# Kernel optimization log

Hardware: AMD Instinct MI355X
Metric: run time of the kernel (lower is better)

Reference implementation:

```python
import jax, jax.numpy as jnp
import numpy as np
import math


def setup_inputs() -> dict:
    key = jax.random.key(0)
    k1, k2, k3 = jax.random.split(key, 3)
    b, h, s, d = 2, 16, 2048, 64
    q = jax.random.normal(k1, (b, h, s, d), dtype=jnp.float32)
    k = jax.random.normal(k2, (b, h, d, s), dtype=jnp.float32)  # pre-transposed as in the torch module
    v = jax.random.normal(k3, (b, h, s, d), dtype=jnp.float32)
    return {"q": q, "k": k, "v": v}


def reference(q, k, v):
    d = q.shape[-1]
    # unnormalized exp-attention, no max subtraction (faithful to source)
    p = jnp.exp(jnp.einsum('bhsd,bhdt->bhst', q, k) / math.sqrt(d))  # [b,h,s,s]
    attn = jnp.einsum('bhst,bhtd->bhsd', p, v)                        # [b,h,s,d]
    l = jnp.sum(p, axis=3, keepdims=True)                             # [b,h,s,1]
    return attn / l
```

## Files before the change

kernel.cpp:

```cpp
#include <hip/hip_runtime.h>

#define S_LEN 2048
#define D_DIM 64
#define BH 32
#define NN ((size_t)131072)

typedef short bf16x8 __attribute__((ext_vector_type(8)));
typedef float f32x16 __attribute__((ext_vector_type(16)));
typedef unsigned int u32x4 __attribute__((ext_vector_type(4)));

static __device__ __forceinline__ unsigned short f2bf(float x) {
  unsigned int u = __float_as_uint(x);
  u += 0x7fffu + ((u >> 16) & 1u);
  return (unsigned short)(u >> 16);
}
static __device__ __forceinline__ float bf2f(unsigned short h) {
  return __uint_as_float(((unsigned int)h) << 16);
}
static __device__ __forceinline__ void gll16(const void* g, void* l) {
  __builtin_amdgcn_global_load_lds((const __attribute__((address_space(1))) void*)g,
                                   (__attribute__((address_space(3))) void*)l, 16, 0, 0);
}

__global__ __launch_bounds__(256) void pack_all(
    const float* __restrict__ kin, const float* __restrict__ vin,
    unsigned short* __restrict__ Kh, unsigned short* __restrict__ Kl,
    unsigned short* __restrict__ Vh) {
  const int gid = blockIdx.x * 256 + threadIdx.x;
  if (gid < 524288) {
    const int bh = gid >> 14, rem = gid & 16383;
    const int u = rem >> 11, t = rem & 2047;
    const float* src = kin + (size_t)bh * 131072 + (size_t)(u * 8) * 2048 + t;
    float x[8];
#pragma unroll
    for (int j = 0; j < 8; ++j) x[j] = src[j * 2048];
    u32x4 hv, lv;
#pragma unroll
    for (int p = 0; p < 4; ++p) {
      unsigned int pk;
      asm("v_cvt_pk_bf16_f32 %0, %1, %2" : "=v"(pk) : "v"(x[2 * p]), "v"(x[2 * p + 1]));
      float l0 = x[2 * p] - __uint_as_float(pk << 16);
      float l1 = x[2 * p + 1] - __uint_as_float(pk & 0xffff0000u);
      unsigned int pl;
      asm("v_cvt_pk_bf16_f32 %0, %1, %2" : "=v"(pl) : "v"(l0), "v"(l1));
      hv[p] = pk;
      lv[p] = pl;
    }
    const size_t o = (size_t)bh * NN + (size_t)(u * 2048 + t) * 8;
    *(u32x4*)(Kh + o) = hv;
    *(u32x4*)(Kl + o) = lv;
  } else {
    const int g2 = gid - 524288;
    const int bh = g2 >> 14, rem = g2 & 16383;
    const int thi = rem >> 6, d = rem & 63;
    const int tr = thi >> 3, u = thi & 7;
    const float* src = vin + (size_t)bh * 131072 + d;
    float x[8];
#pragma unroll
    for (int j = 0; j < 8; ++j) {
      int t = tr * 64 + (u >> 1) * 16 + (u & 1) * 4 + (j & 3) + 8 * (j >> 2);
      x[j] = src[(size_t)t * 64];
    }
    u32x4 hv;
#pragma unroll
    for (int p = 0; p < 4; ++p) {
      unsigned int pk;
      asm("v_cvt_pk_bf16_f32 %0, %1, %2" : "=v"(pk) : "v"(x[2 * p]), "v"(x[2 * p + 1]));
      hv[p] = pk;
    }
    *(u32x4*)(Vh + (size_t)bh * NN + (size_t)(thi * 64 + d) * 8) = hv;
  }
}

__global__ __launch_bounds__(512, 4) void attn_fused(
    const float* __restrict__ q, const unsigned short* __restrict__ Khg,
    const unsigned short* __restrict__ Klg, const unsigned short* __restrict__ Vhg,
    float* __restrict__ out) {
  __shared__ __align__(16) unsigned short smem[2][12288];

  const int bid = blockIdx.x;
  const int swz = (bid & 7) * 64 + (bid >> 3);
  const int bh = swz >> 4;
  const int qt = swz & 15;
  const int tid = threadIdx.x;
  const int w = tid >> 6;
  const int lane = tid & 63;
  const int l31 = lane & 31;
  const int h = lane >> 5;
  const int qtile = w >> 1;
  const int kh2 = w & 1;

  bf16x8 qh[4], ql[4];
  {
    const float* qb = q + ((size_t)bh * S_LEN + qt * 128 + qtile * 32 + l31) * 64;
#pragma unroll
    for (int ks = 0; ks < 4; ++ks) {
      const float* p = qb + ks * 16 + h * 8;
      float4 x0 = *(const float4*)p;
      float4 x1 = *(const float4*)(p + 4);
      float xs[8] = {x0.x, x0.y, x0.z, x0.w, x1.x, x1.y, x1.z, x1.w};
      bf16x8 hh, ll;
#pragma unroll
      for (int j = 0; j < 8; ++j) {
        unsigned short hb = f2bf(xs[j]);
        hh[j] = (short)hb;
        ll[j] = (short)f2bf(xs[j] - bf2f(hb));
      }
      qh[ks] = hh; ql[ks] = ll;
    }
  }

  const unsigned short* srcp[3];
  int stp[3], ldso[3];
#pragma unroll
  for (int i = 0; i < 3; ++i) {
    int g = w * 3 + i;
    int c = g & 7, typ = g >> 3;
    if (typ < 2) {
      size_t off = ((size_t)((c >> 1) * 2 + h) * 2048 + (c & 1) * 32 + l31) * 8;
      srcp[i] = (typ == 0 ? Khg : Klg) + (size_t)bh * NN + off;
      stp[i] = 512;
      ldso[i] = typ * 4096 + c * 512;
    } else {
      size_t off = ((size_t)((c >> 1) * 2 + h) * 64 + (c & 1) * 32 + l31) * 8;
      srcp[i] = Vhg + (size_t)bh * NN + off;
      stp[i] = 4096;
      ldso[i] = 8192 + c * 512;
    }
  }
  auto stage = [&](int buf, int tile) {
#pragma unroll
    for (int i = 0; i < 3; ++i)
      gll16(srcp[i] + (size_t)tile * stp[i], &smem[buf][ldso[i]]);
  };

  f32x16 o2[2] = {};
  float lsum = 0.f;
  const char* lp = (const char*)&smem[0][0] + lane * 16;

  stage(0, 0);
  __syncthreads();

  auto body = [&](int kt, int buf) {
    if (kt < 31) stage(buf ^ 1, kt + 1);
    const char* B = lp + buf * 24576;
    f32x16 acc = {};
    __builtin_amdgcn_s_setprio(1);
#pragma unroll
    for (int ks = 0; ks < 4; ++ks) {
      bf16x8 kh = *(const bf16x8*)(B + (ks * 2 + kh2) * 1024);
      bf16x8 kl = *(const bf16x8*)(B + 8192 + (ks * 2 + kh2) * 1024);
      acc = __builtin_amdgcn_mfma_f32_32x32x16_bf16(kh, qh[ks], acc, 0, 0, 0);
      acc = __builtin_amdgcn_mfma_f32_32x32x16_bf16(kh, ql[ks], acc, 0, 0, 0);
      acc = __builtin_amdgcn_mfma_f32_32x32x16_bf16(kl, qh[ks], acc, 0, 0, 0);
    }
    __builtin_amdgcn_s_setprio(0);
    float pr[16];
#pragma unroll
    for (int i = 0; i < 16; ++i) {
      pr[i] = exp2f(acc[i] * 0.18033688011112042f);
      lsum += pr[i];
    }
    bf16x8 pa[2];
#pragma unroll
    for (int s2 = 0; s2 < 2; ++s2) {
      u32x4 wds;
#pragma unroll
      for (int p2 = 0; p2 < 4; ++p2) {
        unsigned int pk;
        asm("v_cvt_pk_bf16_f32 %0, %1, %2"
            : "=v"(pk)
            : "v"(pr[s2 * 8 + p2 * 2]), "v"(pr[s2 * 8 + p2 * 2 + 1]));
        wds[p2] = pk;
      }
      pa[s2] = __builtin_bit_cast(bf16x8, wds);
    }
    __builtin_amdgcn_s_setprio(1);
#pragma unroll
    for (int db = 0; db < 2; ++db) {
      bf16x8 v0 = *(const bf16x8*)(B + 16384 + ((kh2 * 2 + 0) * 2 + db) * 1024);
      bf16x8 v1 = *(const bf16x8*)(B + 16384 + ((kh2 * 2 + 1) * 2 + db) * 1024);
      o2[db] = __builtin_amdgcn_mfma_f32_32x32x16_bf16(pa[0], v0, o2[db], 0, 0, 0);
      o2[db] = __builtin_amdgcn_mfma_f32_32x32x16_bf16(pa[1], v1, o2[db], 0, 0, 0);
    }
    __builtin_amdgcn_s_setprio(0);
    __syncthreads();
  };

  for (int kt = 0; kt < 32; kt += 2) {
    body(kt, 0);
    body(kt + 1, 1);
  }

  float ls = lsum + __shfl_xor(lsum, 32);
  float* sc = (float*)&smem[0][0];
  if (kh2 == 1) {
#pragma unroll
    for (int db = 0; db < 2; ++db)
#pragma unroll
      for (int r = 0; r < 16; ++r)
        sc[(qtile * 2 + db) * 1024 + (h * 16 + r) * 32 + l31] = o2[db][r];
    sc[8192 + qtile * 32 + l31] = ls;
  }
  __syncthreads();
  if (kh2 == 1) return;
  float ltot = ls + sc[8192 + qtile * 32 + l31];
  float inv = 1.0f / ltot;
  sc[8320 + qtile * 32 + l31] = inv;
  asm volatile("s_waitcnt lgkmcnt(0)" ::: "memory");
  float* ob = out + ((size_t)bh * S_LEN + qt * 128 + qtile * 32) * 64;
#pragma unroll
  for (int r = 0; r < 16; ++r) {
    const int qr = (r & 3) + 8 * (r >> 2) + 4 * h;
    float iv = sc[8320 + qtile * 32 + qr];
#pragma unroll
    for (int db = 0; db < 2; ++db) {
      float val = (o2[db][r] + sc[(qtile * 2 + db) * 1024 + (h * 16 + r) * 32 + l31]) * iv;
      ob[(size_t)qr * 64 + db * 32 + l31] = val;
    }
  }
}

extern "C" void kernel_launch(void* const* d_in, const int* in_sizes, int n_in,
                              void* d_out, int out_size, void* d_ws, size_t ws_size,
                              hipStream_t stream) {
  const float* q = (const float*)d_in[0];
  const float* k = (const float*)d_in[1];
  const float* v = (const float*)d_in[2];
  float* out = (float*)d_out;
  unsigned short* ws = (unsigned short*)d_ws;
  unsigned short* Kh = ws;
  unsigned short* Kl = ws + BH * NN;
  unsigned short* Vh = ws + 2 * BH * NN;
  pack_all<<<dim3(4096), 256, 0, stream>>>(k, v, Kh, Kl, Vh);
  attn_fused<<<dim3(512), 512, 0, stream>>>(q, Kh, Kl, Vh, out);
}
```

Baseline: 161.6 us.

## Triple-buffer K/V tiles with explicit vmcnt waits and raw barriers

Grows LDS staging from two to three buffers so each tile is prefetched two iterations ahead. Replaces __syncthreads with explicit s_waitcnt vmcnt(3) plus s_barrier, so waves wait only on the older in-flight loads. The aim is to hide global-load latency behind the MFMA work. It raises LDS use to 72KB per block, which may reduce occupancy below the 4 blocks per CU requested by the launch bounds.

```diff
diff --git a/kernel.cpp b/kernel.cpp
--- a/kernel.cpp
+++ b/kernel.cpp
@@ -76,7 +76,7 @@
     const float* __restrict__ q, const unsigned short* __restrict__ Khg,
     const unsigned short* __restrict__ Klg, const unsigned short* __restrict__ Vhg,
     float* __restrict__ out) {
-  __shared__ __align__(16) unsigned short smem[2][12288];
+  __shared__ __align__(16) unsigned short smem[3][12288];
 
   const int bid = blockIdx.x;
   const int swz = (bid & 7) * 64 + (bid >> 3);
@@ -138,12 +138,8 @@
   float lsum = 0.f;
   const char* lp = (const char*)&smem[0][0] + lane * 16;
 
-  stage(0, 0);
-  __syncthreads();
-
-  auto body = [&](int kt, int buf) {
-    if (kt < 31) stage(buf ^ 1, kt + 1);
-    const char* B = lp + buf * 24576;
+  auto compute = [&](int bufc) {
+    const char* B = lp + bufc * 24576;
     f32x16 acc = {};
     __builtin_amdgcn_s_setprio(1);
 #pragma unroll
@@ -184,13 +180,33 @@
       o2[db] = __builtin_amdgcn_mfma_f32_32x32x16_bf16(pa[1], v1, o2[db], 0, 0, 0);
     }
     __builtin_amdgcn_s_setprio(0);
-    __syncthreads();
   };
 
-  for (int kt = 0; kt < 32; kt += 2) {
-    body(kt, 0);
-    body(kt + 1, 1);
-  }
+  stage(0, 0);
+  stage(1, 1);
+  asm volatile("s_waitcnt vmcnt(3)" ::: "memory");
+  __builtin_amdgcn_s_barrier();
+
+#pragma unroll 1
+  for (int tb = 0; tb < 30; tb += 3) {
+    stage(2, tb + 2);
+    compute(0);
+    asm volatile("s_waitcnt vmcnt(3) lgkmcnt(0)" ::: "memory");
+    __builtin_amdgcn_s_barrier();
+    stage(0, tb + 3);
+    compute(1);
+    asm volatile("s_waitcnt vmcnt(3) lgkmcnt(0)" ::: "memory");
+    __builtin_amdgcn_s_barrier();
+    stage(1, tb + 4);
+    compute(2);
+    asm volatile("s_waitcnt vmcnt(3) lgkmcnt(0)" ::: "memory");
+    __builtin_amdgcn_s_barrier();
+  }
+  compute(0);
+  asm volatile("s_waitcnt vmcnt(0) lgkmcnt(0)" ::: "memory");
+  __builtin_amdgcn_s_barrier();
+  compute(1);
+  __syncthreads();
 
   float ls = lsum + __shfl_xor(lsum, 32);
   float* sc = (float*)&smem[0][0];
```

Measured after the change: 165.2 us. 1.02x slower.
